# Kernel optimization log

Hardware: AMD Instinct MI355X
Metric: run time of the kernel (lower is better)

## Reference

```python
import jax, jax.numpy as jnp
import numpy as np

N = 200000   # nodes
E = 3200000  # edges
B = 128      # graphs
IN, HID, OUT, C = 768, 64, 64, 4


def gcn_conv(x, src, dst, W, b, n):
    """PyG GCNConv: add self-loops, symmetric deg^-1/2 normalization, linear, scatter-add."""
    xw = x @ W  # [n, out]
    loop = jnp.arange(n)
    s = jnp.concatenate([src, loop])
    d = jnp.concatenate([dst, loop])
    deg = jax.ops.segment_sum(jnp.ones(s.shape, xw.dtype), d, num_segments=n)
    dinv = jnp.where(deg > 0, jax.lax.rsqrt(jnp.maximum(deg, 1e-12)), 0.0)
    norm = dinv[s] * dinv[d]  # [E+n]
    out = jax.ops.segment_sum(norm[:, None] * xw[s], d, num_segments=n)
    return out + b


def rumor_branch(x, src, dst, root, rootindex, batch, W1, b1, W2, b2):
    h = gcn_conv(x, src, dst, W1, b1, N)          # [N, HID]
    x2 = h
    root_extend1 = root[batch]                     # per-node root raw features [N, IN]
    h = jax.nn.relu(jnp.concatenate([h, root_extend1], axis=1))
    # dropout is identity in eval mode
    h = gcn_conv(h, src, dst, W2, b2, N)           # [N, OUT]
    h = jax.nn.relu(h)
    root_extend2 = x2[rootindex][batch]            # [N, HID]
    h = jnp.concatenate([h, root_extend2], axis=1) # [N, OUT+HID]
    sums = jax.ops.segment_sum(h, batch, num_segments=B)
    cnt = jax.ops.segment_sum(jnp.ones((N,), h.dtype), batch, num_segments=B)
    return sums / jnp.maximum(cnt, 1.0)[:, None]   # scatter_mean -> [B, OUT+HID]


def setup_inputs() -> dict:
    key = jax.random.key(0)
    ks = jax.random.split(key, 12)
    return {
        "x": jax.random.normal(ks[0], (N, IN), jnp.float32),
        "edge_index": jax.random.randint(ks[1], (2, E), 0, N, jnp.int64),
        "bu_edge_index": jax.random.randint(ks[2], (2, E), 0, N, jnp.int64),
        "batch": jnp.sort(jax.random.randint(ks[3], (N,), 0, B, jnp.int64)),
        "rootindex": jax.random.randint(ks[4], (B,), 0, N, jnp.int64),
        "root": jax.random.normal(ks[5], (B, IN), jnp.float32),
        "W1_td": jax.random.normal(ks[6], (IN, HID), jnp.float32) * 0.05,
        "b1_td": jnp.zeros((HID,), jnp.float32),
        "W2_td": jax.random.normal(ks[7], (HID + IN, OUT), jnp.float32) * 0.05,
        "b2_td": jnp.zeros((OUT,), jnp.float32),
        "W1_bu": jax.random.normal(ks[8], (IN, HID), jnp.float32) * 0.05,
        "b1_bu": jnp.zeros((HID,), jnp.float32),
        "W2_bu": jax.random.normal(ks[9], (HID + IN, OUT), jnp.float32) * 0.05,
        "b2_bu": jnp.zeros((OUT,), jnp.float32),
        "fc_W": jax.random.normal(ks[10], (2 * (OUT + HID), C), jnp.float32) * 0.05,
        "fc_b": jnp.zeros((C,), jnp.float32),
    }


def reference(x, edge_index, bu_edge_index, batch, rootindex, root,
              W1_td, b1_td, W2_td, b2_td, W1_bu, b1_bu, W2_bu, b2_bu, fc_W, fc_b):
    td = rumor_branch(x, edge_index[0], edge_index[1], root, rootindex, batch,
                      W1_td, b1_td, W2_td, b2_td)
    bu = rumor_branch(x, bu_edge_index[0], bu_edge_index[1], root, rootindex, batch,
                      W1_bu, b1_bu, W2_bu, b2_bu)
    feat = jnp.concatenate([bu, td], axis=1)       # [B, 2*(OUT+HID)]
    logits = feat @ fc_W + fc_b                    # [B, C]
    return jax.nn.log_softmax(logits, axis=1)
```

## Files before the change

### kernel.cpp

```cpp
#include <hip/hip_runtime.h>
#include <math.h>

#define N_NODES 200000
#define N_EDGES 3200000
#define NB      128
#define FIN     768
#define FH      64
#define NC      4

#define SCAN_TILE 1024
#define NBLK ((N_NODES + SCAN_TILE - 1) / SCAN_TILE)

__device__ __forceinline__ unsigned short f2bf(float f) {
    unsigned int u = __float_as_uint(f);
    u += 0x7fffu + ((u >> 16) & 1u);
    return (unsigned short)(u >> 16);
}
__device__ __forceinline__ ushort4 pack4(float4 v) {
    ushort4 h;
    h.x = f2bf(v.x); h.y = f2bf(v.y); h.z = f2bf(v.z); h.w = f2bf(v.w);
    return h;
}
__device__ __forceinline__ float4 unpack4(ushort4 h) {
    float4 f;
    f.x = __uint_as_float((unsigned int)h.x << 16);
    f.y = __uint_as_float((unsigned int)h.y << 16);
    f.z = __uint_as_float((unsigned int)h.z << 16);
    f.w = __uint_as_float((unsigned int)h.w << 16);
    return f;
}

__global__ __launch_bounds__(256) void k_degi(const int* __restrict__ dst_td,
                                              const int* __restrict__ dst_bu,
                                              int* __restrict__ degi) {
    int i = blockIdx.x * blockDim.x + threadIdx.x;
    if (i < N_EDGES) {
        atomicAdd(degi + dst_td[i], 1);
        atomicAdd(degi + N_NODES + dst_bu[i], 1);
    }
}

__global__ __launch_bounds__(256) void k_dinv(const int* __restrict__ degi,
                                              float* __restrict__ dv) {
    int i = blockIdx.x * blockDim.x + threadIdx.x;
    if (i < 2 * N_NODES) dv[i] = rsqrtf((float)degi[i] + 1.0f);
}

__global__ __launch_bounds__(256) void k_scanA(const int* __restrict__ deg,
                                               int* __restrict__ bsum) {
    __shared__ int sh[256];
    int t = threadIdx.x, b = blockIdx.x;
    int base = b * SCAN_TILE + t * 4;
    int s = 0;
#pragma unroll
    for (int j = 0; j < 4; ++j) {
        int idx = base + j;
        if (idx < N_NODES) s += deg[idx];
    }
    sh[t] = s;
    __syncthreads();
    for (int off = 128; off > 0; off >>= 1) {
        if (t < off) sh[t] += sh[t + off];
        __syncthreads();
    }
    if (t == 0) bsum[b] = sh[0];
}

__global__ __launch_bounds__(256) void k_scanB(const int* __restrict__ bsum,
                                               int* __restrict__ boff) {
    __shared__ int sh[256];
    int t = threadIdx.x;
    int v = (t < NBLK) ? bsum[t] : 0;
    sh[t] = v;
    __syncthreads();
    for (int off = 1; off < 256; off <<= 1) {
        int a = (t >= off) ? sh[t - off] : 0;
        __syncthreads();
        sh[t] += a;
        __syncthreads();
    }
    if (t < NBLK) boff[t] = sh[t] - v;
}

__global__ __launch_bounds__(256) void k_scanC(const int* __restrict__ deg,
                                               const int* __restrict__ boff,
                                               int* __restrict__ rowptr,
                                               int* __restrict__ cursor) {
    __shared__ int sh[256];
    int t = threadIdx.x, b = blockIdx.x;
    int base = b * SCAN_TILE + t * 4;
    int v[4];
    int tot = 0;
#pragma unroll
    for (int j = 0; j < 4; ++j) {
        int idx = base + j;
        v[j] = (idx < N_NODES) ? deg[idx] : 0;
        tot += v[j];
    }
    sh[t] = tot;
    __syncthreads();
    for (int off = 1; off < 256; off <<= 1) {
        int a = (t >= off) ? sh[t - off] : 0;
        __syncthreads();
        sh[t] += a;
        __syncthreads();
    }
    int run = boff[b] + sh[t] - tot;
#pragma unroll
    for (int j = 0; j < 4; ++j) {
        int idx = base + j;
        if (idx < N_NODES) {
            rowptr[idx] = run;
            cursor[idx] = run;
            run += v[j];
        }
    }
    if (b == 0 && t == 0) rowptr[N_NODES] = N_EDGES;
}

__global__ __launch_bounds__(256) void k_fill(const int* __restrict__ src,
                                              const int* __restrict__ dst,
                                              int* __restrict__ cursor,
                                              int* __restrict__ csr) {
    int e = blockIdx.x * blockDim.x + threadIdx.x;
    if (e < N_EDGES) {
        int d = dst[e];
        int pos = atomicAdd(cursor + d, 1);
        csr[pos] = src[e];
    }
}

__global__ __launch_bounds__(256) void k_gemm1(const float* __restrict__ x,
                                               const float* __restrict__ Wtd,
                                               const float* __restrict__ Wbu,
                                               const float* __restrict__ dinvtd,
                                               const float* __restrict__ dinvbu,
                                               unsigned short* __restrict__ XWtd,
                                               unsigned short* __restrict__ XWbu) {
    __shared__ __align__(16) float As[16][64];
    __shared__ __align__(16) float Ws[16][128];
    const int tid  = threadIdx.x;
    const int row0 = blockIdx.x * 64;
    const int c0 = (tid & 31) * 4;
    const int r0 = (tid >> 5) * 8;
    const int ar  = tid >> 2;
    const int ak  = (tid & 3) << 2;
    const int asw = (tid & 3) << 3;

    float acc[8][4];
#pragma unroll
    for (int i = 0; i < 8; ++i)
#pragma unroll
        for (int j = 0; j < 4; ++j) acc[i][j] = 0.f;

    for (int k0 = 0; k0 < FIN; k0 += 16) {
        float4 av = *(const float4*)(x + (size_t)(row0 + ar) * FIN + k0 + ak);
        float4 wv[2];
#pragma unroll
        for (int t2 = 0; t2 < 2; ++t2) {
            int f  = tid * 2 + t2;
            int kk = f >> 5;
            int c  = (f & 31) << 2;
            const float* Wp = (c < 64) ? (Wtd + (size_t)(k0 + kk) * 64 + c)
                                       : (Wbu + (size_t)(k0 + kk) * 64 + (c - 64));
            wv[t2] = *(const float4*)Wp;
        }
        {
            int sc = ar ^ asw;
            As[ak + 0][sc] = av.x;
            As[ak + 1][sc] = av.y;
            As[ak + 2][sc] = av.z;
            As[ak + 3][sc] = av.w;
        }
#pragma unroll
        for (int t2 = 0; t2 < 2; ++t2) {
            int f  = tid * 2 + t2;
            int kk = f >> 5;
            int c  = (f & 31) << 2;
            *(float4*)&Ws[kk][c] = wv[t2];
        }
        __syncthreads();
#pragma unroll
        for (int kk = 0; kk < 16; ++kk) {
            int sw = ((kk >> 2) & 3) << 3;
            float a[8];
            *(float4*)&a[0] = *(const float4*)&As[kk][(r0) ^ sw];
            *(float4*)&a[4] = *(const float4*)&As[kk][(r0 + 4) ^ sw];
            float4 w = *(const float4*)&Ws[kk][c0];
#pragma unroll
            for (int i = 0; i < 8; ++i) {
                acc[i][0] = fmaf(a[i], w.x, acc[i][0]);
                acc[i][1] = fmaf(a[i], w.y, acc[i][1]);
                acc[i][2] = fmaf(a[i], w.z, acc[i][2]);
                acc[i][3] = fmaf(a[i], w.w, acc[i][3]);
            }
        }
        __syncthreads();
    }
    const int cc = c0 & 63;
    unsigned short* outb   = (c0 < 64) ? XWtd   : XWbu;
    const float*    dvp    = (c0 < 64) ? dinvtd : dinvbu;
#pragma unroll
    for (int i = 0; i < 8; ++i) {
        int row = row0 + r0 + i;
        float dv = dvp[row];
        float4 v = make_float4(acc[i][0] * dv, acc[i][1] * dv,
                               acc[i][2] * dv, acc[i][3] * dv);
        *(ushort4*)(outb + (size_t)row * 64 + cc) = pack4(v);
    }
}

__global__ __launch_bounds__(128) void k_rb(const float* __restrict__ root,
                                            const float* __restrict__ W2td,
                                            const float* __restrict__ W2bu,
                                            float* __restrict__ RBtd,
                                            float* __restrict__ RBbu) {
    int b = blockIdx.x;
    int c = threadIdx.x;
    const float* W2 = (c < 64) ? W2td : W2bu;
    int cc = c & 63;
    const float* rp = root + (size_t)b * FIN;
    float s = 0.f;
    for (int k = 0; k < FIN; ++k) {
        float r = fmaxf(rp[k], 0.f);
        s = fmaf(r, W2[(size_t)(64 + k) * 64 + cc], s);
    }
    (c < 64 ? RBtd : RBbu)[b * 64 + cc] = s;
}

__global__ __launch_bounds__(256) void k_gather(const int* __restrict__ rowptr,
                                                const int* __restrict__ csr,
                                                const float* __restrict__ dinv,
                                                const unsigned short* __restrict__ xh,
                                                const float* __restrict__ bias,
                                                float* __restrict__ out) {
    int t    = blockIdx.x * blockDim.x + threadIdx.x;
    int node = t >> 4;
    int li   = (t & 15) << 2;
    if (node >= N_NODES) return;
    float4 acc0 = unpack4(*(const ushort4*)(xh + (size_t)node * 64 + li));
    float4 acc1 = make_float4(0.f, 0.f, 0.f, 0.f);
    int e0 = rowptr[node], e1 = rowptr[node + 1];
    int e = e0;
    for (; e + 4 <= e1; e += 4) {
        int s0 = csr[e + 0], s1 = csr[e + 1], s2 = csr[e + 2], s3 = csr[e + 3];
        float4 v0 = unpack4(*(const ushort4*)(xh + (size_t)s0 * 64 + li));
        float4 v1 = unpack4(*(const ushort4*)(xh + (size_t)s1 * 64 + li));
        float4 v2 = unpack4(*(const ushort4*)(xh + (size_t)s2 * 64 + li));
        float4 v3 = unpack4(*(const ushort4*)(xh + (size_t)s3 * 64 + li));
        acc0.x += (v0.x + v1.x) + (v2.x + v3.x);
        acc0.y += (v0.y + v1.y) + (v2.y + v3.y);
        acc0.z += (v0.z + v1.z) + (v2.z + v3.z);
        acc0.w += (v0.w + v1.w) + (v2.w + v3.w);
    }
    for (; e < e1; ++e) {
        int s = csr[e];
        float4 v = unpack4(*(const ushort4*)(xh + (size_t)s * 64 + li));
        acc1.x += v.x; acc1.y += v.y; acc1.z += v.z; acc1.w += v.w;
    }
    acc0.x += acc1.x; acc0.y += acc1.y; acc0.z += acc1.z; acc0.w += acc1.w;
    float dv = dinv[node];
    float4 bb = *(const float4*)(bias + li);
    float4 r;
    r.x = fmaf(dv, acc0.x, bb.x);
    r.y = fmaf(dv, acc0.y, bb.y);
    r.z = fmaf(dv, acc0.z, bb.z);
    r.w = fmaf(dv, acc0.w, bb.w);
    *(float4*)(out + (size_t)node * 64 + li) = r;
}

__global__ __launch_bounds__(256) void k_gemm2(const float* __restrict__ H1,
                                               const float* __restrict__ W2,
                                               const float* __restrict__ RB,
                                               const int* __restrict__ batch,
                                               const float* __restrict__ dinv,
                                               unsigned short* __restrict__ XW2) {
    __shared__ __align__(16) float As[16][64];
    __shared__ __align__(16) float Ws[16][64];
    const int tid  = threadIdx.x;
    const int row0 = blockIdx.x * 64;
    const int c0 = (tid & 15) * 4;
    const int r0 = (tid >> 4) * 4;
    float acc[4][4];
#pragma unroll
    for (int i = 0; i < 4; ++i)
#pragma unroll
        for (int j = 0; j < 4; ++j) acc[i][j] = 0.f;

    const int ar  = tid >> 2;
    const int ak  = (tid & 3) << 2;
    const int asw = (tid & 3) << 3;
    const int wk  = tid >> 4;
    const int wc  = (tid & 15) << 2;

    for (int k0 = 0; k0 < FH; k0 += 16) {
        float4 av = *(const float4*)(H1 + (size_t)(row0 + ar) * 64 + k0 + ak);
        int sc = ar ^ asw;
        As[ak + 0][sc] = fmaxf(av.x, 0.f);
        As[ak + 1][sc] = fmaxf(av.y, 0.f);
        As[ak + 2][sc] = fmaxf(av.z, 0.f);
        As[ak + 3][sc] = fmaxf(av.w, 0.f);
        *(float4*)&Ws[wk][wc] = *(const float4*)(W2 + (size_t)(k0 + wk) * 64 + wc);
        __syncthreads();
#pragma unroll
        for (int kk = 0; kk < 16; ++kk) {
            int sw = ((kk >> 2) & 3) << 3;
            float4 w = *(float4*)&Ws[kk][c0];
            float4 a = *(const float4*)&As[kk][r0 ^ sw];
            acc[0][0] = fmaf(a.x, w.x, acc[0][0]); acc[0][1] = fmaf(a.x, w.y, acc[0][1]);
            acc[0][2] = fmaf(a.x, w.z, acc[0][2]); acc[0][3] = fmaf(a.x, w.w, acc[0][3]);
            acc[1][0] = fmaf(a.y, w.x, acc[1][0]); acc[1][1] = fmaf(a.y, w.y, acc[1][1]);
            acc[1][2] = fmaf(a.y, w.z, acc[1][2]); acc[1][3] = fmaf(a.y, w.w, acc[1][3]);
            acc[2][0] = fmaf(a.z, w.x, acc[2][0]); acc[2][1] = fmaf(a.z, w.y, acc[2][1]);
            acc[2][2] = fmaf(a.z, w.z, acc[2][2]); acc[2][3] = fmaf(a.z, w.w, acc[2][3]);
            acc[3][0] = fmaf(a.w, w.x, acc[3][0]); acc[3][1] = fmaf(a.w, w.y, acc[3][1]);
            acc[3][2] = fmaf(a.w, w.z, acc[3][2]); acc[3][3] = fmaf(a.w, w.w, acc[3][3]);
        }
        __syncthreads();
    }
#pragma unroll
    for (int i = 0; i < 4; ++i) {
        int row = row0 + r0 + i;
        int bg  = batch[row];
        float dv = dinv[row];
        float4 rb = *(const float4*)(RB + (size_t)bg * 64 + c0);
        float4 xw2 = make_float4((acc[i][0] + rb.x) * dv, (acc[i][1] + rb.y) * dv,
                                 (acc[i][2] + rb.z) * dv, (acc[i][3] + rb.w) * dv);
        *(ushort4*)(XW2 + (size_t)row * 64 + c0) = pack4(xw2);
    }
}

__device__ __forceinline__ int lb_search(const int* __restrict__ a, int n, int v) {
    int lo = 0, hi = n;
    while (lo < hi) {
        int m = (lo + hi) >> 1;
        if (a[m] < v) lo = m + 1; else hi = m;
    }
    return lo;
}

__global__ __launch_bounds__(512) void k_pool(const float* __restrict__ H2,
                                              const float* __restrict__ H1,
                                              const int* __restrict__ batch,
                                              const int* __restrict__ rootindex,
                                              float* __restrict__ pooled) {
    int b    = blockIdx.x;
    int lane = threadIdx.x & 63;
    int wv   = threadIdx.x >> 6;
    int start = lb_search(batch, N_NODES, b);
    int end   = lb_search(batch, N_NODES, b + 1);
    float acc = 0.f;
    for (int i = start + wv; i < end; i += 8)
        acc += fmaxf(H2[(size_t)i * 64 + lane], 0.f);
    __shared__ float red[8][64];
    red[wv][lane] = acc;
    __syncthreads();
    if (wv == 0) {
        float s = 0.f;
#pragma unroll
        for (int w = 0; w < 8; ++w) s += red[w][lane];
        int cnt = end - start;
        float inv = 1.0f / fmaxf((float)cnt, 1.0f);
        pooled[b * 128 + lane] = s * inv;
        float rootv = (cnt > 0) ? H1[(size_t)rootindex[b] * 64 + lane] : 0.f;
        pooled[b * 128 + 64 + lane] = rootv;
    }
}

__global__ __launch_bounds__(128) void k_final(const float* __restrict__ ptd,
                                               const float* __restrict__ pbu,
                                               const float* __restrict__ fcW,
                                               const float* __restrict__ fcb,
                                               float* __restrict__ out) {
    int b = threadIdx.x;
    if (b >= NB) return;
    float l[4] = {fcb[0], fcb[1], fcb[2], fcb[3]};
    for (int j = 0; j < 256; ++j) {
        float f = (j < 128) ? pbu[b * 128 + j] : ptd[b * 128 + (j - 128)];
#pragma unroll
        for (int c = 0; c < 4; ++c) l[c] = fmaf(f, fcW[j * 4 + c], l[c]);
    }
    float m = fmaxf(fmaxf(l[0], l[1]), fmaxf(l[2], l[3]));
    float s = expf(l[0] - m) + expf(l[1] - m) + expf(l[2] - m) + expf(l[3] - m);
    float ls = logf(s);
#pragma unroll
    for (int c = 0; c < 4; ++c) out[b * 4 + c] = l[c] - m - ls;
}

extern "C" void kernel_launch(void* const* d_in, const int* in_sizes, int n_in,
                              void* d_out, int out_size, void* d_ws, size_t ws_size,
                              hipStream_t stream) {
    const float* x     = (const float*)d_in[0];
    const int*   ei    = (const int*)d_in[1];
    const int*   bei   = (const int*)d_in[2];
    const int*   batch = (const int*)d_in[3];
    const int*   rooti = (const int*)d_in[4];
    const float* root  = (const float*)d_in[5];
    const float* W1td  = (const float*)d_in[6];
    const float* b1td  = (const float*)d_in[7];
    const float* W2td  = (const float*)d_in[8];
    const float* b2td  = (const float*)d_in[9];
    const float* W1bu  = (const float*)d_in[10];
    const float* b1bu  = (const float*)d_in[11];
    const float* W2bu  = (const float*)d_in[12];
    const float* b2bu  = (const float*)d_in[13];
    const float* fcW   = (const float*)d_in[14];
    const float* fcb   = (const float*)d_in[15];
    float* out = (float*)d_out;

    char* ws = (char*)d_ws;
    size_t o = 0;
    const size_t NF = (size_t)N_NODES * 64;
    auto alloc_f = [&](size_t n) { float* p = (float*)(ws + o); o += n * 4; return p; };
    auto alloc_h = [&](size_t n) { unsigned short* p = (unsigned short*)(ws + o); o += n * 2; return p; };
    auto alloc_i = [&](size_t n) { int*   p = (int*)  (ws + o); o += n * 4; return p; };

    unsigned short* XWtd = alloc_h(NF);
    unsigned short* XWbu = alloc_h(NF);
    float* H1     = alloc_f(NF);
    float* H2     = alloc_f(NF);
    float* dinvtd = alloc_f(N_NODES);
    float* dinvbu = alloc_f(N_NODES);
    float* RBtd   = alloc_f((size_t)NB * 64);
    float* RBbu   = alloc_f((size_t)NB * 64);
    float* pooltd = alloc_f((size_t)NB * 128);
    float* poolbu = alloc_f((size_t)NB * 128);
    int* degi     = alloc_i(2 * (size_t)N_NODES);
    int* rp_td    = alloc_i(N_NODES + 1);
    int* rp_bu    = alloc_i(N_NODES + 1);
    int* cur_td   = alloc_i(N_NODES);
    int* cur_bu   = alloc_i(N_NODES);
    int* bsum     = alloc_i(256);
    int* boff     = alloc_i(256);
    int* csr_td   = alloc_i(N_EDGES);
    int* csr_bu   = alloc_i(N_EDGES);

    const int eb = (N_EDGES + 255) / 256;

    hipMemsetAsync(degi, 0, 2 * (size_t)N_NODES * sizeof(int), stream);
    k_degi<<<eb, 256, 0, stream>>>(ei + N_EDGES, bei + N_EDGES, degi);
    k_dinv<<<(2 * N_NODES + 255) / 256, 256, 0, stream>>>(degi, dinvtd);

    k_scanA<<<NBLK, 256, 0, stream>>>(degi, bsum);
    k_scanB<<<1, 256, 0, stream>>>(bsum, boff);
    k_scanC<<<NBLK, 256, 0, stream>>>(degi, boff, rp_td, cur_td);
    k_fill<<<eb, 256, 0, stream>>>(ei, ei + N_EDGES, cur_td, csr_td);

    k_scanA<<<NBLK, 256, 0, stream>>>(degi + N_NODES, bsum);
    k_scanB<<<1, 256, 0, stream>>>(bsum, boff);
    k_scanC<<<NBLK, 256, 0, stream>>>(degi + N_NODES, boff, rp_bu, cur_bu);
    k_fill<<<eb, 256, 0, stream>>>(bei, bei + N_EDGES, cur_bu, csr_bu);

    k_gemm1<<<N_NODES / 64, 256, 0, stream>>>(x, W1td, W1bu, dinvtd, dinvbu, XWtd, XWbu);
    k_rb<<<NB, 128, 0, stream>>>(root, W2td, W2bu, RBtd, RBbu);

    const int gb = (N_NODES * 16) / 256;

    k_gather<<<gb, 256, 0, stream>>>(rp_td, csr_td, dinvtd, XWtd, b1td, H1);
    k_gemm2<<<N_NODES / 64, 256, 0, stream>>>(H1, W2td, RBtd, batch, dinvtd, XWtd );
    k_gather<<<gb, 256, 0, stream>>>(rp_td, csr_td, dinvtd, XWtd, b2td, H2);
    k_pool<<<NB, 512, 0, stream>>>(H2, H1, batch, rooti, pooltd);

    k_gather<<<gb, 256, 0, stream>>>(rp_bu, csr_bu, dinvbu, XWbu, b1bu, H1);
    k_gemm2<<<N_NODES / 64, 256, 0, stream>>>(H1, W2bu, RBbu, batch, dinvbu, XWbu );
    k_gather<<<gb, 256, 0, stream>>>(rp_bu, csr_bu, dinvbu, XWbu, b2bu, H2);
    k_pool<<<NB, 512, 0, stream>>>(H2, H1, batch, rooti, poolbu);

    k_final<<<1, 128, 0, stream>>>(pooltd, poolbu, fcW, fcb, out);
}
```

Before: 2.502 ms.

## Use fp16 MFMA for first GEMM and merge td/bu branch kernels with fused pooling

The first-layer GEMM now runs on fp16 MFMA 16x16x32 instructions, reading weights from a pre-packed fp16 buffer instead of doing fp32 FMA through shared memory. The td and bu branches are merged into single launches for the CSR fill, the first gather, gemm2 and the second gather. The second gather is fused with ReLU and mean-pool partial sums through a shared-memory segmented reduction plus atomics, which removes the H2 buffer and the separate pool kernel. This cuts launch count and memory traffic, but fp16 inputs lower GEMM precision and the float atomics make the pooled sums non-deterministic.

```diff
diff --git a/kernel.cpp b/kernel.cpp
--- a/kernel.cpp
+++ b/kernel.cpp
@@ -7,19 +7,20 @@
 #define FIN     768
 #define FH      64
 #define NC      4
+#define GB      12500
+#define NB2     (N_NODES / 64)
 
 #define SCAN_TILE 1024
 #define NBLK ((N_NODES + SCAN_TILE - 1) / SCAN_TILE)
+
+typedef _Float16 f16;
+typedef __attribute__((ext_vector_type(8))) _Float16 f16x8;
+typedef __attribute__((ext_vector_type(4))) float f32x4;
 
 __device__ __forceinline__ unsigned short f2bf(float f) {
     unsigned int u = __float_as_uint(f);
     u += 0x7fffu + ((u >> 16) & 1u);
     return (unsigned short)(u >> 16);
-}
-__device__ __forceinline__ ushort4 pack4(float4 v) {
-    ushort4 h;
-    h.x = f2bf(v.x); h.y = f2bf(v.y); h.z = f2bf(v.z); h.w = f2bf(v.w);
-    return h;
 }
 __device__ __forceinline__ float4 unpack4(ushort4 h) {
     float4 f;
@@ -118,95 +119,115 @@
     if (b == 0 && t == 0) rowptr[N_NODES] = N_EDGES;
 }
 
-__global__ __launch_bounds__(256) void k_fill(const int* __restrict__ src,
-                                              const int* __restrict__ dst,
-                                              int* __restrict__ cursor,
-                                              int* __restrict__ csr) {
-    int e = blockIdx.x * blockDim.x + threadIdx.x;
+__global__ __launch_bounds__(256) void k_fill2(const int* __restrict__ ei,
+                                               const int* __restrict__ bei,
+                                               int* __restrict__ cur_td,
+                                               int* __restrict__ cur_bu,
+                                               int* __restrict__ csr_td,
+                                               int* __restrict__ csr_bu) {
+    int i = blockIdx.x * blockDim.x + threadIdx.x;
+    int e = (i >= N_EDGES) ? i - N_EDGES : i;
+    const int* src = (i >= N_EDGES) ? bei : ei;
+    int* cursor    = (i >= N_EDGES) ? cur_bu : cur_td;
+    int* csr       = (i >= N_EDGES) ? csr_bu : csr_td;
     if (e < N_EDGES) {
-        int d = dst[e];
+        int d = src[N_EDGES + e];
         int pos = atomicAdd(cursor + d, 1);
         csr[pos] = src[e];
     }
 }
 
+__global__ __launch_bounds__(256) void k_wpack(const float* __restrict__ Wtd,
+                                               const float* __restrict__ Wbu,
+                                               f16* __restrict__ Wp) {
+    int tid = blockIdx.x * 256 + threadIdx.x;
+    if (tid >= 8 * 24 * 64) return;
+    int c  = tid / (24 * 64);
+    int kb = (tid / 64) % 24;
+    int l  = tid & 63;
+    int col = c * 16 + (l & 15);
+    int k0  = kb * 32 + (l >> 4) * 8;
+    const float* Wsrc = (col < 64) ? (Wtd + col) : (Wbu + (col - 64));
+    f16 v[8];
+#pragma unroll
+    for (int i = 0; i < 8; ++i) v[i] = (f16)Wsrc[(size_t)(k0 + i) * 64];
+    *(f16x8*)(Wp + (size_t)tid * 8) = *(f16x8*)v;
+}
+
 __global__ __launch_bounds__(256) void k_gemm1(const float* __restrict__ x,
-                                               const float* __restrict__ Wtd,
-                                               const float* __restrict__ Wbu,
+                                               const f16* __restrict__ Wp,
                                                const float* __restrict__ dinvtd,
                                                const float* __restrict__ dinvbu,
                                                unsigned short* __restrict__ XWtd,
                                                unsigned short* __restrict__ XWbu) {
-    __shared__ __align__(16) float As[16][64];
-    __shared__ __align__(16) float Ws[16][128];
-    const int tid  = threadIdx.x;
-    const int row0 = blockIdx.x * 64;
-    const int c0 = (tid & 31) * 4;
-    const int r0 = (tid >> 5) * 8;
-    const int ar  = tid >> 2;
-    const int ak  = (tid & 3) << 2;
-    const int asw = (tid & 3) << 3;
-
-    float acc[8][4];
-#pragma unroll
-    for (int i = 0; i < 8; ++i)
-#pragma unroll
-        for (int j = 0; j < 4; ++j) acc[i][j] = 0.f;
-
-    for (int k0 = 0; k0 < FIN; k0 += 16) {
-        float4 av = *(const float4*)(x + (size_t)(row0 + ar) * FIN + k0 + ak);
-        float4 wv[2];
-#pragma unroll
-        for (int t2 = 0; t2 < 2; ++t2) {
-            int f  = tid * 2 + t2;
-            int kk = f >> 5;
-            int c  = (f & 31) << 2;
-            const float* Wp = (c < 64) ? (Wtd + (size_t)(k0 + kk) * 64 + c)
-                                       : (Wbu + (size_t)(k0 + kk) * 64 + (c - 64));
-            wv[t2] = *(const float4*)Wp;
-        }
-        {
-            int sc = ar ^ asw;
-            As[ak + 0][sc] = av.x;
-            As[ak + 1][sc] = av.y;
-            As[ak + 2][sc] = av.z;
-            As[ak + 3][sc] = av.w;
-        }
-#pragma unroll
-        for (int t2 = 0; t2 < 2; ++t2) {
-            int f  = tid * 2 + t2;
-            int kk = f >> 5;
-            int c  = (f & 31) << 2;
-            *(float4*)&Ws[kk][c] = wv[t2];
-        }
-        __syncthreads();
-#pragma unroll
-        for (int kk = 0; kk < 16; ++kk) {
-            int sw = ((kk >> 2) & 3) << 3;
-            float a[8];
-            *(float4*)&a[0] = *(const float4*)&As[kk][(r0) ^ sw];
-            *(float4*)&a[4] = *(const float4*)&As[kk][(r0 + 4) ^ sw];
-            float4 w = *(const float4*)&Ws[kk][c0];
-#pragma unroll
-            for (int i = 0; i < 8; ++i) {
-                acc[i][0] = fmaf(a[i], w.x, acc[i][0]);
-                acc[i][1] = fmaf(a[i], w.y, acc[i][1]);
-                acc[i][2] = fmaf(a[i], w.z, acc[i][2]);
-                acc[i][3] = fmaf(a[i], w.w, acc[i][3]);
+    const int tid = threadIdx.x;
+    const int wv  = tid >> 6;
+    const int l   = tid & 63;
+    const int lr  = l & 15;
+    const int lh  = l >> 4;
+    const int row_base = blockIdx.x * 128 + wv * 32;
+
+    const float* xr[2];
+#pragma unroll
+    for (int rt = 0; rt < 2; ++rt) {
+        int ar = row_base + rt * 16 + lr;
+        if (ar > N_NODES - 1) ar = N_NODES - 1;
+        xr[rt] = x + (size_t)ar * FIN + lh * 8;
+    }
+
+    f32x4 acc[2][8];
+#pragma unroll
+    for (int rt = 0; rt < 2; ++rt)
+#pragma unroll
+        for (int c = 0; c < 8; ++c) acc[rt][c] = (f32x4){0.f, 0.f, 0.f, 0.f};
+
+    float4 na0[2], na1[2];
+#pragma unroll
+    for (int rt = 0; rt < 2; ++rt) {
+        na0[rt] = *(const float4*)(xr[rt]);
+        na1[rt] = *(const float4*)(xr[rt] + 4);
+    }
+
+    for (int kb = 0; kb < 24; ++kb) {
+        f16x8 af[2];
+#pragma unroll
+        for (int rt = 0; rt < 2; ++rt) {
+            float4 c0 = na0[rt], c1 = na1[rt];
+            af[rt][0] = (f16)c0.x; af[rt][1] = (f16)c0.y;
+            af[rt][2] = (f16)c0.z; af[rt][3] = (f16)c0.w;
+            af[rt][4] = (f16)c1.x; af[rt][5] = (f16)c1.y;
+            af[rt][6] = (f16)c1.z; af[rt][7] = (f16)c1.w;
+        }
+        if (kb < 23) {
+#pragma unroll
+            for (int rt = 0; rt < 2; ++rt) {
+                na0[rt] = *(const float4*)(xr[rt] + (kb + 1) * 32);
+                na1[rt] = *(const float4*)(xr[rt] + (kb + 1) * 32 + 4);
             }
         }
-        __syncthreads();
-    }
-    const int cc = c0 & 63;
-    unsigned short* outb   = (c0 < 64) ? XWtd   : XWbu;
-    const float*    dvp    = (c0 < 64) ? dinvtd : dinvbu;
-#pragma unroll
-    for (int i = 0; i < 8; ++i) {
-        int row = row0 + r0 + i;
-        float dv = dvp[row];
-        float4 v = make_float4(acc[i][0] * dv, acc[i][1] * dv,
-                               acc[i][2] * dv, acc[i][3] * dv);
-        *(ushort4*)(outb + (size_t)row * 64 + cc) = pack4(v);
+        const f16* wb = Wp + ((size_t)kb * 64 + l) * 8;
+#pragma unroll
+        for (int c = 0; c < 8; ++c) {
+            f16x8 bf = *(const f16x8*)(wb + (size_t)c * (24 * 64 * 8));
+            acc[0][c] = __builtin_amdgcn_mfma_f32_16x16x32_f16(af[0], bf, acc[0][c], 0, 0, 0);
+            acc[1][c] = __builtin_amdgcn_mfma_f32_16x16x32_f16(af[1], bf, acc[1][c], 0, 0, 0);
+        }
+    }
+#pragma unroll
+    for (int rt = 0; rt < 2; ++rt) {
+#pragma unroll
+        for (int j = 0; j < 4; ++j) {
+            int r = row_base + rt * 16 + lh * 4 + j;
+            if (r < N_NODES) {
+                float dtd = dinvtd[r], dbu = dinvbu[r];
+#pragma unroll
+                for (int c = 0; c < 8; ++c) {
+                    float v = acc[rt][c][j] * (c < 4 ? dtd : dbu);
+                    unsigned short* ob = (c < 4) ? XWtd : XWbu;
+                    ob[(size_t)r * 64 + (c & 3) * 16 + lr] = f2bf(v);
+                }
+            }
+        }
     }
 }
 
@@ -228,16 +249,30 @@
     (c < 64 ? RBtd : RBbu)[b * 64 + cc] = s;
 }
 
-__global__ __launch_bounds__(256) void k_gather(const int* __restrict__ rowptr,
-                                                const int* __restrict__ csr,
-                                                const float* __restrict__ dinv,
-                                                const unsigned short* __restrict__ xh,
-                                                const float* __restrict__ bias,
-                                                float* __restrict__ out) {
-    int t    = blockIdx.x * blockDim.x + threadIdx.x;
+__global__ __launch_bounds__(256) void k_gather1(const int* __restrict__ rp_td,
+                                                 const int* __restrict__ csr_td,
+                                                 const int* __restrict__ rp_bu,
+                                                 const int* __restrict__ csr_bu,
+                                                 const float* __restrict__ dinvtd,
+                                                 const float* __restrict__ dinvbu,
+                                                 const unsigned short* __restrict__ XWtd,
+                                                 const unsigned short* __restrict__ XWbu,
+                                                 const float* __restrict__ b1td,
+                                                 const float* __restrict__ b1bu,
+                                                 float* __restrict__ H1td,
+                                                 float* __restrict__ H1bu) {
+    const bool bu = blockIdx.x >= GB;
+    const int bid = bu ? blockIdx.x - GB : blockIdx.x;
+    const int* rowptr = bu ? rp_bu : rp_td;
+    const int* csr    = bu ? csr_bu : csr_td;
+    const float* dinv = bu ? dinvbu : dinvtd;
+    const unsigned short* xh = bu ? XWbu : XWtd;
+    const float* bias = bu ? b1bu : b1td;
+    float* out        = bu ? H1bu : H1td;
+
+    int t    = bid * blockDim.x + threadIdx.x;
     int node = t >> 4;
     int li   = (t & 15) << 2;
-    if (node >= N_NODES) return;
     float4 acc0 = unpack4(*(const ushort4*)(xh + (size_t)node * 64 + li));
     float4 acc1 = make_float4(0.f, 0.f, 0.f, 0.f);
     int e0 = rowptr[node], e1 = rowptr[node + 1];
@@ -269,16 +304,29 @@
     *(float4*)(out + (size_t)node * 64 + li) = r;
 }
 
-__global__ __launch_bounds__(256) void k_gemm2(const float* __restrict__ H1,
-                                               const float* __restrict__ W2,
-                                               const float* __restrict__ RB,
+__global__ __launch_bounds__(256) void k_gemm2(const float* __restrict__ H1td,
+                                               const float* __restrict__ H1bu,
+                                               const float* __restrict__ W2td,
+                                               const float* __restrict__ W2bu,
+                                               const float* __restrict__ RBtd,
+                                               const float* __restrict__ RBbu,
                                                const int* __restrict__ batch,
-                                               const float* __restrict__ dinv,
-                                               unsigned short* __restrict__ XW2) {
+                                               const float* __restrict__ dinvtd,
+                                               const float* __restrict__ dinvbu,
+                                               unsigned short* __restrict__ XW2td,
+                                               unsigned short* __restrict__ XW2bu) {
+    const bool bu = blockIdx.x >= NB2;
+    const int bid = bu ? blockIdx.x - NB2 : blockIdx.x;
+    const float* H1  = bu ? H1bu : H1td;
+    const float* W2  = bu ? W2bu : W2td;
+    const float* RB  = bu ? RBbu : RBtd;
+    const float* dinv = bu ? dinvbu : dinvtd;
+    unsigned short* XW2 = bu ? XW2bu : XW2td;
+
     __shared__ __align__(16) float As[16][64];
     __shared__ __align__(16) float Ws[16][64];
     const int tid  = threadIdx.x;
-    const int row0 = blockIdx.x * 64;
+    const int row0 = bid * 64;
     const int c0 = (tid & 15) * 4;
     const int r0 = (tid >> 4) * 4;
     float acc[4][4];
@@ -324,9 +372,84 @@
         int bg  = batch[row];
         float dv = dinv[row];
         float4 rb = *(const float4*)(RB + (size_t)bg * 64 + c0);
-        float4 xw2 = make_float4((acc[i][0] + rb.x) * dv, (acc[i][1] + rb.y) * dv,
-                                 (acc[i][2] + rb.z) * dv, (acc[i][3] + rb.w) * dv);
-        *(ushort4*)(XW2 + (size_t)row * 64 + c0) = pack4(xw2);
+        float v0 = (acc[i][0] + rb.x) * dv, v1 = (acc[i][1] + rb.y) * dv;
+        float v2 = (acc[i][2] + rb.z) * dv, v3 = (acc[i][3] + rb.w) * dv;
+        ushort4 h; h.x = f2bf(v0); h.y = f2bf(v1); h.z = f2bf(v2); h.w = f2bf(v3);
+        *(ushort4*)(XW2 + (size_t)row * 64 + c0) = h;
+    }
+}
+
+__global__ __launch_bounds__(256) void k_g2pool(const int* __restrict__ rp_td,
+                                                const int* __restrict__ csr_td,
+                                                const int* __restrict__ rp_bu,
+                                                const int* __restrict__ csr_bu,
+                                                const float* __restrict__ dinvtd,
+                                                const float* __restrict__ dinvbu,
+                                                const unsigned short* __restrict__ XW2td,
+                                                const unsigned short* __restrict__ XW2bu,
+                                                const float* __restrict__ b2td,
+                                                const float* __restrict__ b2bu,
+                                                const int* __restrict__ batch,
+                                                float* __restrict__ poolsum) {
+    const bool bu = blockIdx.x >= GB;
+    const int bid = bu ? blockIdx.x - GB : blockIdx.x;
+    const int* rowptr = bu ? rp_bu : rp_td;
+    const int* csr    = bu ? csr_bu : csr_td;
+    const float* dinv = bu ? dinvbu : dinvtd;
+    const unsigned short* xh = bu ? XW2bu : XW2td;
+    const float* bias = bu ? b2bu : b2td;
+    float* ps = poolsum + (bu ? NB * 64 : 0);
+
+    int t    = bid * blockDim.x + threadIdx.x;
+    int node = t >> 4;
+    int li   = (t & 15) << 2;
+    float4 acc0 = unpack4(*(const ushort4*)(xh + (size_t)node * 64 + li));
+    int e0 = rowptr[node], e1 = rowptr[node + 1];
+    int e = e0;
+    for (; e + 4 <= e1; e += 4) {
+        int s0 = csr[e + 0], s1 = csr[e + 1], s2 = csr[e + 2], s3 = csr[e + 3];
+        float4 v0 = unpack4(*(const ushort4*)(xh + (size_t)s0 * 64 + li));
+        float4 v1 = unpack4(*(const ushort4*)(xh + (size_t)s1 * 64 + li));
+        float4 v2 = unpack4(*(const ushort4*)(xh + (size_t)s2 * 64 + li));
+        float4 v3 = unpack4(*(const ushort4*)(xh + (size_t)s3 * 64 + li));
+        acc0.x += (v0.x + v1.x) + (v2.x + v3.x);
+        acc0.y += (v0.y + v1.y) + (v2.y + v3.y);
+        acc0.z += (v0.z + v1.z) + (v2.z + v3.z);
+        acc0.w += (v0.w + v1.w) + (v2.w + v3.w);
+    }
+    for (; e < e1; ++e) {
+        int s = csr[e];
+        float4 v = unpack4(*(const ushort4*)(xh + (size_t)s * 64 + li));
+        acc0.x += v.x; acc0.y += v.y; acc0.z += v.z; acc0.w += v.w;
+    }
+    float dv = dinv[node];
+    float4 bb = *(const float4*)(bias + li);
+    float4 r;
+    r.x = fmaxf(fmaf(dv, acc0.x, bb.x), 0.f);
+    r.y = fmaxf(fmaf(dv, acc0.y, bb.y), 0.f);
+    r.z = fmaxf(fmaf(dv, acc0.z, bb.z), 0.f);
+    r.w = fmaxf(fmaf(dv, acc0.w, bb.w), 0.f);
+
+    __shared__ __align__(16) float red[16][72];
+    __shared__ int bat[16];
+    int slot = threadIdx.x >> 4;
+    *(float4*)&red[slot][li] = r;
+    if ((threadIdx.x & 15) == 0) bat[slot] = batch[node];
+    __syncthreads();
+    if (threadIdx.x < 64) {
+        int c = threadIdx.x;
+        float run = red[0][c];
+        int cur = bat[0];
+        for (int i = 1; i < 16; ++i) {
+            int bi = bat[i];
+            if (bi != cur) {
+                atomicAdd(&ps[cur * 64 + c], run);
+                run = 0.f;
+                cur = bi;
+            }
+            run += red[i][c];
+        }
+        atomicAdd(&ps[cur * 64 + c], run);
     }
 }
 
@@ -339,44 +462,28 @@
     return lo;
 }
 
-__global__ __launch_bounds__(512) void k_pool(const float* __restrict__ H2,
-                                              const float* __restrict__ H1,
-                                              const int* __restrict__ batch,
-                                              const int* __restrict__ rootindex,
-                                              float* __restrict__ pooled) {
-    int b    = blockIdx.x;
-    int lane = threadIdx.x & 63;
-    int wv   = threadIdx.x >> 6;
-    int start = lb_search(batch, N_NODES, b);
-    int end   = lb_search(batch, N_NODES, b + 1);
-    float acc = 0.f;
-    for (int i = start + wv; i < end; i += 8)
-        acc += fmaxf(H2[(size_t)i * 64 + lane], 0.f);
-    __shared__ float red[8][64];
-    red[wv][lane] = acc;
-    __syncthreads();
-    if (wv == 0) {
-        float s = 0.f;
-#pragma unroll
-        for (int w = 0; w < 8; ++w) s += red[w][lane];
-        int cnt = end - start;
-        float inv = 1.0f / fmaxf((float)cnt, 1.0f);
-        pooled[b * 128 + lane] = s * inv;
-        float rootv = (cnt > 0) ? H1[(size_t)rootindex[b] * 64 + lane] : 0.f;
-        pooled[b * 128 + 64 + lane] = rootv;
-    }
-}
-
-__global__ __launch_bounds__(128) void k_final(const float* __restrict__ ptd,
-                                               const float* __restrict__ pbu,
+__global__ __launch_bounds__(128) void k_final(const float* __restrict__ poolsum,
+                                               const float* __restrict__ H1td,
+                                               const float* __restrict__ H1bu,
+                                               const int* __restrict__ batch,
+                                               const int* __restrict__ rooti,
                                                const float* __restrict__ fcW,
                                                const float* __restrict__ fcb,
                                                float* __restrict__ out) {
     int b = threadIdx.x;
     if (b >= NB) return;
+    int start = lb_search(batch, N_NODES, b);
+    int end   = lb_search(batch, N_NODES, b + 1);
+    int cnt   = end - start;
+    float inv = 1.0f / fmaxf((float)cnt, 1.0f);
+    int ri = rooti[b];
     float l[4] = {fcb[0], fcb[1], fcb[2], fcb[3]};
     for (int j = 0; j < 256; ++j) {
-        float f = (j < 128) ? pbu[b * 128 + j] : ptd[b * 128 + (j - 128)];
+        float f;
+        if (j < 64)       f = poolsum[NB * 64 + b * 64 + j] * inv;
+        else if (j < 128) f = (cnt > 0) ? H1bu[(size_t)ri * 64 + (j - 64)] : 0.f;
+        else if (j < 192) f = poolsum[b * 64 + (j - 128)] * inv;
+        else              f = (cnt > 0) ? H1td[(size_t)ri * 64 + (j - 192)] : 0.f;
 #pragma unroll
         for (int c = 0; c < 4; ++c) l[c] = fmaf(f, fcW[j * 4 + c], l[c]);
     }
@@ -417,14 +524,14 @@
 
     unsigned short* XWtd = alloc_h(NF);
     unsigned short* XWbu = alloc_h(NF);
-    float* H1     = alloc_f(NF);
-    float* H2     = alloc_f(NF);
+    float* H1td   = alloc_f(NF);
+    float* H1bu   = alloc_f(NF);
+    f16*   Wp     = (f16*)alloc_h(8 * 24 * 64 * 8);
     float* dinvtd = alloc_f(N_NODES);
     float* dinvbu = alloc_f(N_NODES);
     float* RBtd   = alloc_f((size_t)NB * 64);
     float* RBbu   = alloc_f((size_t)NB * 64);
-    float* pooltd = alloc_f((size_t)NB * 128);
-    float* poolbu = alloc_f((size_t)NB * 128);
+    float* poolsum = alloc_f(2 * (size_t)NB * 64);
     int* degi     = alloc_i(2 * (size_t)N_NODES);
     int* rp_td    = alloc_i(N_NODES + 1);
     int* rp_bu    = alloc_i(N_NODES + 1);
@@ -437,6 +544,8 @@
 
     const int eb = (N_EDGES + 255) / 256;
 
+    k_wpack<<<48, 256, 0, stream>>>(W1td, W1bu, Wp);
+
     hipMemsetAsync(degi, 0, 2 * (size_t)N_NODES * sizeof(int), stream);
     k_degi<<<eb, 256, 0, stream>>>(ei + N_EDGES, bei + N_EDGES, degi);
     k_dinv<<<(2 * N_NODES + 255) / 256, 256, 0, stream>>>(degi, dinvtd);
@@ -444,27 +553,22 @@
     k_scanA<<<NBLK, 256, 0, stream>>>(degi, bsum);
     k_scanB<<<1, 256, 0, stream>>>(bsum, boff);
     k_scanC<<<NBLK, 256, 0, stream>>>(degi, boff, rp_td, cur_td);
-    k_fill<<<eb, 256, 0, stream>>>(ei, ei + N_EDGES, cur_td, csr_td);
-
     k_scanA<<<NBLK, 256, 0, stream>>>(degi + N_NODES, bsum);
     k_scanB<<<1, 256, 0, stream>>>(bsum, boff);
     k_scanC<<<NBLK, 256, 0, stream>>>(degi + N_NODES, boff, rp_bu, cur_bu);
-    k_fill<<<eb, 256, 0, stream>>>(bei, bei + N_EDGES, cur_bu, csr_bu);
-
-    k_gemm1<<<N_NODES / 64, 256, 0, stream>>>(x, W1td, W1bu, dinvtd, dinvbu, XWtd, XWbu);
+    k_fill2<<<2 * eb, 256, 0, stream>>>(ei, bei, cur_td, cur_bu, csr_td, csr_bu);
+
+    k_gemm1<<<(N_NODES + 127) / 128, 256, 0, stream>>>(x, Wp, dinvtd, dinvbu, XWtd, XWbu);
     k_rb<<<NB, 128, 0, stream>>>(root, W2td, W2bu, RBtd, RBbu);
-
-    const int gb = (N_NODES * 16) / 256;
-
-    k_gather<<<gb, 256, 0, stream>>>(rp_td, csr_td, dinvtd, XWtd, b1td, H1);
-    k_gemm2<<<N_NODES / 64, 256, 0, stream>>>(H1, W2td, RBtd, batch, dinvtd, XWtd );
-    k_gather<<<gb, 256, 0, stream>>>(rp_td, csr_td, dinvtd, XWtd, b2td, H2);
-    k_pool<<<NB, 512, 0, stream>>>(H2, H1, batch, rooti, pooltd);
-
-    k_gather<<<gb, 256, 0, stream>>>(rp_bu, csr_bu, dinvbu, XWbu, b1bu, H1);
-    k_gemm2<<<N_NODES / 64, 256, 0, stream>>>(H1, W2bu, RBbu, batch, dinvbu, XWbu );
-    k_gather<<<gb, 256, 0, stream>>>(rp_bu, csr_bu, dinvbu, XWbu, b2bu, H2);
-    k_pool<<<NB, 512, 0, stream>>>(H2, H1, batch, rooti, poolbu);
-
-    k_final<<<1, 128, 0, stream>>>(pooltd, poolbu, fcW, fcb, out);
-}
+    hipMemsetAsync(poolsum, 0, 2 * (size_t)NB * 64 * sizeof(float), stream);
+
+    k_gather1<<<2 * GB, 256, 0, stream>>>(rp_td, csr_td, rp_bu, csr_bu,
+                                          dinvtd, dinvbu, XWtd, XWbu,
+                                          b1td, b1bu, H1td, H1bu);
+    k_gemm2<<<2 * NB2, 256, 0, stream>>>(H1td, H1bu, W2td, W2bu, RBtd, RBbu,
+                                         batch, dinvtd, dinvbu, XWtd, XWbu);
+    k_g2pool<<<2 * GB, 256, 0, stream>>>(rp_td, csr_td, rp_bu, csr_bu,
+                                         dinvtd, dinvbu, XWtd, XWbu,
+                                         b2td, b2bu, batch, poolsum);
+    k_final<<<1, 128, 0, stream>>>(poolsum, H1td, H1bu, batch, rooti, fcW, fcb, out);
+}
```

New measurement: 2.119 ms. 15.3% less time.
